# Kernel tuning notes

Hardware: AMD Instinct MI355X
Metric: run time of the kernel (lower is better)

The kernel has to match this reference:

```python
import jax, jax.numpy as jnp
import numpy as np

B, T, D, H = 512, 256, 64, 64  # batch, seq_len, input_dim, hidden_dim


def _lstm_params(key, in_dim, hid):
    k = 1.0 / np.sqrt(hid)
    k1, k2, k3, k4 = jax.random.split(key, 4)
    W_ih = jax.random.uniform(k1, (4 * hid, in_dim), jnp.float32, -k, k)
    W_hh = jax.random.uniform(k2, (4 * hid, hid), jnp.float32, -k, k)
    b_ih = jax.random.uniform(k3, (4 * hid,), jnp.float32, -k, k)
    b_hh = jax.random.uniform(k4, (4 * hid,), jnp.float32, -k, k)
    return W_ih, W_hh, b_ih, b_hh


def setup_inputs() -> dict:
    key = jax.random.key(0)
    ks = jax.random.split(key, 5)
    inp = {"x": jax.random.normal(ks[0], (B, T, D), jnp.float32)}
    names = ["enc0", "enc1", "dec0", "dec1"]
    # encoder: D->H, H->H ; decoder: H->D, D->D (decoder hidden size = input_dim)
    dims = [(D, H), (H, H), (H, D), (D, D)]
    for name, (i, h), k in zip(names, dims, ks[1:]):
        W_ih, W_hh, b_ih, b_hh = _lstm_params(k, i, h)
        inp[f"{name}_Wih"] = W_ih
        inp[f"{name}_Whh"] = W_hh
        inp[f"{name}_bih"] = b_ih
        inp[f"{name}_bhh"] = b_hh
    return inp


def lstm_layer(x, W_ih, W_hh, b_ih, b_hh):
    # x: [B, T, in]; PyTorch gate order: i, f, g, o
    b = x.shape[0]
    h_dim = W_hh.shape[1]
    # precompute input contribution for all timesteps (one big GEMM)
    xg = jnp.einsum('bti,gi->btg', x, W_ih) + b_ih + b_hh  # [B, T, 4H]

    def step(carry, xt):
        h, c = carry
        g = xt + h @ W_hh.T  # [B, 4H]
        i, f, gg, o = jnp.split(g, 4, axis=-1)
        i = jax.nn.sigmoid(i)
        f = jax.nn.sigmoid(f)
        gg = jnp.tanh(gg)
        o = jax.nn.sigmoid(o)
        c = f * c + i * gg
        h = o * jnp.tanh(c)
        return (h, c), h

    h0 = jnp.zeros((b, h_dim), x.dtype)
    (_, _), hs = jax.lax.scan(step, (h0, h0), jnp.swapaxes(xg, 0, 1))
    return jnp.swapaxes(hs, 0, 1)  # [B, T, H]


def reference(x,
              enc0_Wih, enc0_Whh, enc0_bih, enc0_bhh,
              enc1_Wih, enc1_Whh, enc1_bih, enc1_bhh,
              dec0_Wih, dec0_Whh, dec0_bih, dec0_bhh,
              dec1_Wih, dec1_Whh, dec1_bih, dec1_bhh):
    # Eval-mode forward (inter-layer dropout p=0.2 is disabled at inference)
    h = lstm_layer(x, enc0_Wih, enc0_Whh, enc0_bih, enc0_bhh)
    enc = lstm_layer(h, enc1_Wih, enc1_Whh, enc1_bih, enc1_bhh)
    h = lstm_layer(enc, dec0_Wih, dec0_Whh, dec0_bih, dec0_bhh)
    dec = lstm_layer(h, dec1_Wih, dec1_Whh, dec1_bih, dec1_bhh)
    return dec
```

## Files before the change

kernel.cpp:

```cpp
#include <hip/hip_runtime.h>


typedef _Float16 f16x8 __attribute__((ext_vector_type(8)));
typedef float    f32x4 __attribute__((ext_vector_type(4)));

#define TSEQ 256

__device__ __forceinline__ float fast_rcp(float x) { return __builtin_amdgcn_rcpf(x); }
__device__ __forceinline__ float sigm(float x) { return fast_rcp(1.0f + __expf(-x)); }
__device__ __forceinline__ float tanh_fast(float x) {
    return 2.0f * fast_rcp(1.0f + __expf(-2.0f * x)) - 1.0f;
}
__device__ __forceinline__ f16x8 cvt8(float4 a, float4 b) {
    f16x8 f;
    f[0] = (_Float16)a.x; f[1] = (_Float16)a.y; f[2] = (_Float16)a.z; f[3] = (_Float16)a.w;
    f[4] = (_Float16)b.x; f[5] = (_Float16)b.y; f[6] = (_Float16)b.z; f[7] = (_Float16)b.w;
    return f;
}
__device__ __forceinline__ float bperm(int addr, float v) {
    return __int_as_float(__builtin_amdgcn_ds_bpermute(addr, __float_as_int(v)));
}

__global__ __launch_bounds__(512, 2)
void lstm_fused12(const float* __restrict__ x,
                  float* __restrict__ out,
                  const float* __restrict__ Wih0, const float* __restrict__ Whh0,
                  const float* __restrict__ bi0,  const float* __restrict__ bh0,
                  const float* __restrict__ Wih1, const float* __restrict__ Whh1,
                  const float* __restrict__ bi1,  const float* __restrict__ bh1,
                  const float* __restrict__ Wih2, const float* __restrict__ Whh2,
                  const float* __restrict__ bi2,  const float* __restrict__ bh2,
                  const float* __restrict__ Wih3, const float* __restrict__ Whh3,
                  const float* __restrict__ bi3,  const float* __restrict__ bh3)
{
    __shared__ _Float16 Hb[4][4][2][64];
    __shared__ int      Sf[8];

    const int tid  = threadIdx.x;
    const int wave = tid >> 6;
    const int lane = tid & 63;
    const int L    = wave >> 1;
    const int mh   = wave & 1;
    const int q    = lane >> 4;
    const int n    = lane & 15;
    const int b0   = blockIdx.x * 2;

    const float* Wih = (L == 0) ? Wih0 : (L == 1) ? Wih1 : (L == 2) ? Wih2 : Wih3;
    const float* Whh = (L == 0) ? Whh0 : (L == 1) ? Whh1 : (L == 2) ? Whh2 : Whh3;
    const float* bi  = (L == 0) ? bi0  : (L == 1) ? bi1  : (L == 2) ? bi2  : bi3;
    const float* bh  = (L == 0) ? bh0  : (L == 1) ? bh1  : (L == 2) ? bh2  : bh3;

    f16x8 Bih[4][2][2], Bhh[4][2][2];
#pragma unroll
    for (int g = 0; g < 4; ++g) {
#pragma unroll
        for (int s = 0; s < 2; ++s) {
            const int row = g * 64 + mh * 32 + s * 16 + n;
#pragma unroll
            for (int c = 0; c < 2; ++c) {
                const float* pi = Wih + row * 64 + c * 32 + q * 8;
                const float* ph = Whh + row * 64 + c * 32 + q * 8;
                f16x8 fi, fh;
#pragma unroll
                for (int k = 0; k < 8; ++k) { fi[k] = (_Float16)pi[k]; fh[k] = (_Float16)ph[k]; }
                Bih[g][s][c] = fi;
                Bhh[g][s][c] = fh;
            }
        }
    }

    const int eu = lane & 31;
    const int el = lane >> 5;
    const int unit = mh * 32 + eu;
    float4 be;
    be.x = bi[unit]       + bh[unit];
    be.y = bi[64 + unit]  + bh[64 + unit];
    be.z = bi[128 + unit] + bh[128 + unit];
    be.w = bi[192 + unit] + bh[192 + unit];
    float cst = 0.0f;
    float* outp = out + ((size_t)(b0 + el) * TSEQ) * 64 + unit;

    const int baddr = n * 4;

    ((int*)Hb)[tid] = 0;
    ((int*)Hb)[tid + 512] = 0;
    if (tid < 8) Sf[tid] = -2;

    const float* xbase = x + ((size_t)(b0 + (n & 1)) * TSEQ) * 64 + q * 8;
    float4 A0, A1, A2, A3, B0, B1, B2, B3;
    A0 = A1 = A2 = A3 = make_float4(0.f, 0.f, 0.f, 0.f);
    B0 = B1 = B2 = B3 = A0;
    if (L == 0 && n < 2) {
        A0 = *(const float4*)(xbase);      A1 = *(const float4*)(xbase + 4);
        A2 = *(const float4*)(xbase + 32); A3 = *(const float4*)(xbase + 36);
        B0 = *(const float4*)(xbase + 64);  B1 = *(const float4*)(xbase + 68);
        B2 = *(const float4*)(xbase + 96);  B3 = *(const float4*)(xbase + 100);
    }

    __syncthreads();

    const f32x4 z4 = {0.f, 0.f, 0.f, 0.f};
    const int NI = 131;

    for (int i = 0; i < NI; ++i) {
        const bool act = (unsigned)(i - L) < 128u;
        if (act) {
            const int s0 = 2 * (i - L);
            const int s1 = s0 + 1;

            f16x8 vfA0, vfA1, vfB0, vfB1;
            if (L == 0) {
                vfA0 = cvt8(A0, A1);  vfA1 = cvt8(A2, A3);
                vfB0 = cvt8(B0, B1);  vfB1 = cvt8(B2, B3);
                if (s0 + 2 < TSEQ && n < 2) {
                    const float* p = xbase + (size_t)(s0 + 2) * 64;
                    A0 = *(const float4*)(p);      A1 = *(const float4*)(p + 4);
                    A2 = *(const float4*)(p + 32); A3 = *(const float4*)(p + 36);
                    if (s0 + 3 < TSEQ) {
                        B0 = *(const float4*)(p + 64); B1 = *(const float4*)(p + 68);
                        B2 = *(const float4*)(p + 96); B3 = *(const float4*)(p + 100);
                    }
                }
            } else {
                const _Float16* va = &Hb[s0 & 3][L - 1][n & 1][0];
                vfA0 = *(const f16x8*)(va + q * 8);
                vfA1 = *(const f16x8*)(va + 32 + q * 8);
                const _Float16* vb = &Hb[s1 & 3][L - 1][n & 1][0];
                vfB0 = *(const f16x8*)(vb + q * 8);
                vfB1 = *(const f16x8*)(vb + 32 + q * 8);
            }
            const _Float16* hp = &Hb[(s0 - 1) & 3][L][n & 1][0];
            f16x8 hf0 = *(const f16x8*)(hp + q * 8);
            f16x8 hf1 = *(const f16x8*)(hp + 32 + q * 8);

            f32x4 Cgs[2][4];
#pragma unroll
            for (int s = 0; s < 2; ++s) {
#pragma unroll
                for (int g = 0; g < 4; ++g) {
                    f32x4 c;
                    c = __builtin_amdgcn_mfma_f32_16x16x32_f16(hf0, Bhh[g][s][0], z4, 0, 0, 0);
                    c = __builtin_amdgcn_mfma_f32_16x16x32_f16(hf1, Bhh[g][s][1], c,  0, 0, 0);
                    c = __builtin_amdgcn_mfma_f32_16x16x32_f16(vfA0, Bih[g][s][0], c,  0, 0, 0);
                    Cgs[s][g] = __builtin_amdgcn_mfma_f32_16x16x32_f16(vfA1, Bih[g][s][1], c, 0, 0, 0);
                }
            }
            float gv[4];
#pragma unroll
            for (int g = 0; g < 4; ++g) {
                float v00 = bperm(baddr, Cgs[0][g][0]);
                float v10 = bperm(baddr, Cgs[1][g][0]);
                float v01 = bperm(baddr, Cgs[0][g][1]);
                float v11 = bperm(baddr, Cgs[1][g][1]);
                float lo = (q & 1) ? v10 : v00;
                float hi = (q & 1) ? v11 : v01;
                gv[g] = (q & 2) ? hi : lo;
            }
            {
                float gi = sigm(gv[0] + be.x);
                float gf = sigm(gv[1] + be.y);
                float gg = tanh_fast(gv[2] + be.z);
                float go = sigm(gv[3] + be.w);
                cst = gf * cst + gi * gg;
                float h = go * tanh_fast(cst);
                if (L == 3) outp[(size_t)s0 * 64] = h;
                Hb[s0 & 3][L][el][unit] = (_Float16)h;
            }

            asm volatile("s_waitcnt lgkmcnt(0)" ::: "memory");
            if (lane == 0) ((volatile int*)Sf)[wave] = s0;
            for (;;) {
                asm volatile("" ::: "memory");
                int pv = ((volatile int*)Sf)[wave ^ 1];
                if (pv >= s0) break;
                __builtin_amdgcn_s_sleep(1);
            }
            const _Float16* hq = &Hb[s0 & 3][L][n & 1][0];
            f16x8 hg0 = *(const f16x8*)(hq + q * 8);
            f16x8 hg1 = *(const f16x8*)(hq + 32 + q * 8);

#pragma unroll
            for (int s = 0; s < 2; ++s) {
#pragma unroll
                for (int g = 0; g < 4; ++g) {
                    f32x4 c;
                    c = __builtin_amdgcn_mfma_f32_16x16x32_f16(hg0, Bhh[g][s][0], z4, 0, 0, 0);
                    c = __builtin_amdgcn_mfma_f32_16x16x32_f16(hg1, Bhh[g][s][1], c,  0, 0, 0);
                    c = __builtin_amdgcn_mfma_f32_16x16x32_f16(vfB0, Bih[g][s][0], c,  0, 0, 0);
                    Cgs[s][g] = __builtin_amdgcn_mfma_f32_16x16x32_f16(vfB1, Bih[g][s][1], c, 0, 0, 0);
                }
            }
#pragma unroll
            for (int g = 0; g < 4; ++g) {
                float v00 = bperm(baddr, Cgs[0][g][0]);
                float v10 = bperm(baddr, Cgs[1][g][0]);
                float v01 = bperm(baddr, Cgs[0][g][1]);
                float v11 = bperm(baddr, Cgs[1][g][1]);
                float lo = (q & 1) ? v10 : v00;
                float hi = (q & 1) ? v11 : v01;
                gv[g] = (q & 2) ? hi : lo;
            }
            {
                float gi = sigm(gv[0] + be.x);
                float gf = sigm(gv[1] + be.y);
                float gg = tanh_fast(gv[2] + be.z);
                float go = sigm(gv[3] + be.w);
                cst = gf * cst + gi * gg;
                float h = go * tanh_fast(cst);
                if (L == 3) outp[(size_t)s1 * 64] = h;
                Hb[s1 & 3][L][el][unit] = (_Float16)h;
            }
        }
        __builtin_amdgcn_sched_barrier(0);
        asm volatile("s_waitcnt lgkmcnt(0)" ::: "memory");
        __builtin_amdgcn_s_barrier();
        __builtin_amdgcn_sched_barrier(0);
    }
}

extern "C" void kernel_launch(void* const* d_in, const int* in_sizes, int n_in,
                              void* d_out, int out_size, void* d_ws, size_t ws_size,
                              hipStream_t stream) {
    const float* x = (const float*)d_in[0];
    float* out = (float*)d_out;

    lstm_fused12<<<256, 512, 0, stream>>>(
        x, out,
        (const float*)d_in[1],  (const float*)d_in[2],
        (const float*)d_in[3],  (const float*)d_in[4],
        (const float*)d_in[5],  (const float*)d_in[6],
        (const float*)d_in[7],  (const float*)d_in[8],
        (const float*)d_in[9],  (const float*)d_in[10],
        (const float*)d_in[11], (const float*)d_in[12],
        (const float*)d_in[13], (const float*)d_in[14],
        (const float*)d_in[15], (const float*)d_in[16]);
}
```

Measured before the change: 385.4 us.

## Pack both timesteps' input projections into one MFMA pass using spare M rows

The 16-row MFMA tile only used rows 0-1 (two batch rows). Rows 2-3 now carry the second timestep's input, so one set of input-projection MFMAs covers both timesteps. The recurrent term for step s1 is then accumulated onto those rows with only the W_hh MFMAs, and rows 2-3 are read back. This removes the input-projection MFMAs from the second half-step, shortening the serial critical path. The cost is extra lane-select logic, zeroed h operands on the extra rows, and a different accumulation order.

```diff
diff --git a/kernel.cpp b/kernel.cpp
--- a/kernel.cpp
+++ b/kernel.cpp
@@ -22,7 +22,7 @@
 }
 
 __global__ __launch_bounds__(512, 2)
-void lstm_fused12(const float* __restrict__ x,
+void lstm_fused13(const float* __restrict__ x,
                   float* __restrict__ out,
                   const float* __restrict__ Wih0, const float* __restrict__ Whh0,
                   const float* __restrict__ bi0,  const float* __restrict__ bh0,
@@ -44,6 +44,7 @@
     const int q    = lane >> 4;
     const int n    = lane & 15;
     const int b0   = blockIdx.x * 2;
+    const int lsel = (n >> 1) == 1;
 
     const float* Wih = (L == 0) ? Wih0 : (L == 1) ? Wih1 : (L == 2) ? Wih2 : Wih3;
     const float* Whh = (L == 0) ? Whh0 : (L == 1) ? Whh1 : (L == 2) ? Whh2 : Whh3;
@@ -87,14 +88,12 @@
     if (tid < 8) Sf[tid] = -2;
 
     const float* xbase = x + ((size_t)(b0 + (n & 1)) * TSEQ) * 64 + q * 8;
-    float4 A0, A1, A2, A3, B0, B1, B2, B3;
-    A0 = A1 = A2 = A3 = make_float4(0.f, 0.f, 0.f, 0.f);
-    B0 = B1 = B2 = B3 = A0;
-    if (L == 0 && n < 2) {
-        A0 = *(const float4*)(xbase);      A1 = *(const float4*)(xbase + 4);
-        A2 = *(const float4*)(xbase + 32); A3 = *(const float4*)(xbase + 36);
-        B0 = *(const float4*)(xbase + 64);  B1 = *(const float4*)(xbase + 68);
-        B2 = *(const float4*)(xbase + 96);  B3 = *(const float4*)(xbase + 100);
+    float4 R0, R1, R2, R3;
+    R0 = R1 = R2 = R3 = make_float4(0.f, 0.f, 0.f, 0.f);
+    if (L == 0 && n < 4) {
+        const float* p = xbase + (size_t)(n >> 1) * 64;
+        R0 = *(const float4*)(p);      R1 = *(const float4*)(p + 4);
+        R2 = *(const float4*)(p + 32); R3 = *(const float4*)(p + 36);
     }
 
     __syncthreads();
@@ -107,31 +106,36 @@
         if (act) {
             const int s0 = 2 * (i - L);
             const int s1 = s0 + 1;
-
-            f16x8 vfA0, vfA1, vfB0, vfB1;
+            const int p2 = (s0 & 3);
+            const int sprev = (s0 - 1) & 3;
+
+            f16x8 vf0, vf1;
             if (L == 0) {
-                vfA0 = cvt8(A0, A1);  vfA1 = cvt8(A2, A3);
-                vfB0 = cvt8(B0, B1);  vfB1 = cvt8(B2, B3);
-                if (s0 + 2 < TSEQ && n < 2) {
-                    const float* p = xbase + (size_t)(s0 + 2) * 64;
-                    A0 = *(const float4*)(p);      A1 = *(const float4*)(p + 4);
-                    A2 = *(const float4*)(p + 32); A3 = *(const float4*)(p + 36);
-                    if (s0 + 3 < TSEQ) {
-                        B0 = *(const float4*)(p + 64); B1 = *(const float4*)(p + 68);
-                        B2 = *(const float4*)(p + 96); B3 = *(const float4*)(p + 100);
+                vf0 = cvt8(R0, R1);
+                vf1 = cvt8(R2, R3);
+                if (n < 4) {
+                    const int tl = s0 + 2 + (n >> 1);
+                    if (tl < TSEQ) {
+                        const float* p = xbase + (size_t)tl * 64;
+                        R0 = *(const float4*)(p);      R1 = *(const float4*)(p + 4);
+                        R2 = *(const float4*)(p + 32); R3 = *(const float4*)(p + 36);
                     }
                 }
             } else {
-                const _Float16* va = &Hb[s0 & 3][L - 1][n & 1][0];
-                vfA0 = *(const f16x8*)(va + q * 8);
-                vfA1 = *(const f16x8*)(va + 32 + q * 8);
-                const _Float16* vb = &Hb[s1 & 3][L - 1][n & 1][0];
-                vfB0 = *(const f16x8*)(vb + q * 8);
-                vfB1 = *(const f16x8*)(vb + 32 + q * 8);
-            }
-            const _Float16* hp = &Hb[(s0 - 1) & 3][L][n & 1][0];
-            f16x8 hf0 = *(const f16x8*)(hp + q * 8);
-            f16x8 hf1 = *(const f16x8*)(hp + 32 + q * 8);
+                const _Float16* vp = &Hb[p2 + lsel][L - 1][n & 1][0];
+                vf0 = *(const f16x8*)(vp + q * 8);
+                vf1 = *(const f16x8*)(vp + 32 + q * 8);
+            }
+            f16x8 hf0, hf1;
+            {
+                const _Float16* hp = &Hb[sprev][L][n & 1][0];
+                hf0 = *(const f16x8*)(hp + q * 8);
+                hf1 = *(const f16x8*)(hp + 32 + q * 8);
+                if (lsel) {
+#pragma unroll
+                    for (int k = 0; k < 8; ++k) { hf0[k] = (_Float16)0.f; hf1[k] = (_Float16)0.f; }
+                }
+            }
 
             f32x4 Cgs[2][4];
 #pragma unroll
@@ -139,12 +143,13 @@
 #pragma unroll
                 for (int g = 0; g < 4; ++g) {
                     f32x4 c;
-                    c = __builtin_amdgcn_mfma_f32_16x16x32_f16(hf0, Bhh[g][s][0], z4, 0, 0, 0);
-                    c = __builtin_amdgcn_mfma_f32_16x16x32_f16(hf1, Bhh[g][s][1], c,  0, 0, 0);
-                    c = __builtin_amdgcn_mfma_f32_16x16x32_f16(vfA0, Bih[g][s][0], c,  0, 0, 0);
-                    Cgs[s][g] = __builtin_amdgcn_mfma_f32_16x16x32_f16(vfA1, Bih[g][s][1], c, 0, 0, 0);
-                }
-            }
+                    c = __builtin_amdgcn_mfma_f32_16x16x32_f16(vf0, Bih[g][s][0], z4, 0, 0, 0);
+                    c = __builtin_amdgcn_mfma_f32_16x16x32_f16(vf1, Bih[g][s][1], c,  0, 0, 0);
+                    c = __builtin_amdgcn_mfma_f32_16x16x32_f16(hf0, Bhh[g][s][0], c,  0, 0, 0);
+                    Cgs[s][g] = __builtin_amdgcn_mfma_f32_16x16x32_f16(hf1, Bhh[g][s][1], c, 0, 0, 0);
+                }
+            }
+
             float gv[4];
 #pragma unroll
             for (int g = 0; g < 4; ++g) {
@@ -164,7 +169,7 @@
                 cst = gf * cst + gi * gg;
                 float h = go * tanh_fast(cst);
                 if (L == 3) outp[(size_t)s0 * 64] = h;
-                Hb[s0 & 3][L][el][unit] = (_Float16)h;
+                Hb[p2][L][el][unit] = (_Float16)h;
             }
 
             asm volatile("s_waitcnt lgkmcnt(0)" ::: "memory");
@@ -175,7 +180,7 @@
                 if (pv >= s0) break;
                 __builtin_amdgcn_s_sleep(1);
             }
-            const _Float16* hq = &Hb[s0 & 3][L][n & 1][0];
+            const _Float16* hq = &Hb[p2][L][n & 1][0];
             f16x8 hg0 = *(const f16x8*)(hq + q * 8);
             f16x8 hg1 = *(const f16x8*)(hq + 32 + q * 8);
 
@@ -184,18 +189,17 @@
 #pragma unroll
                 for (int g = 0; g < 4; ++g) {
                     f32x4 c;
-                    c = __builtin_amdgcn_mfma_f32_16x16x32_f16(hg0, Bhh[g][s][0], z4, 0, 0, 0);
-                    c = __builtin_amdgcn_mfma_f32_16x16x32_f16(hg1, Bhh[g][s][1], c,  0, 0, 0);
-                    c = __builtin_amdgcn_mfma_f32_16x16x32_f16(vfB0, Bih[g][s][0], c,  0, 0, 0);
-                    Cgs[s][g] = __builtin_amdgcn_mfma_f32_16x16x32_f16(vfB1, Bih[g][s][1], c, 0, 0, 0);
-                }
-            }
+                    c = __builtin_amdgcn_mfma_f32_16x16x32_f16(hg0, Bhh[g][s][0], Cgs[s][g], 0, 0, 0);
+                    Cgs[s][g] = __builtin_amdgcn_mfma_f32_16x16x32_f16(hg1, Bhh[g][s][1], c, 0, 0, 0);
+                }
+            }
+
 #pragma unroll
             for (int g = 0; g < 4; ++g) {
-                float v00 = bperm(baddr, Cgs[0][g][0]);
-                float v10 = bperm(baddr, Cgs[1][g][0]);
-                float v01 = bperm(baddr, Cgs[0][g][1]);
-                float v11 = bperm(baddr, Cgs[1][g][1]);
+                float v00 = bperm(baddr, Cgs[0][g][2]);
+                float v10 = bperm(baddr, Cgs[1][g][2]);
+                float v01 = bperm(baddr, Cgs[0][g][3]);
+                float v11 = bperm(baddr, Cgs[1][g][3]);
                 float lo = (q & 1) ? v10 : v00;
                 float hi = (q & 1) ? v11 : v01;
                 gv[g] = (q & 2) ? hi : lo;
@@ -208,7 +212,7 @@
                 cst = gf * cst + gi * gg;
                 float h = go * tanh_fast(cst);
                 if (L == 3) outp[(size_t)s1 * 64] = h;
-                Hb[s1 & 3][L][el][unit] = (_Float16)h;
+                Hb[p2 + 1][L][el][unit] = (_Float16)h;
             }
         }
         __builtin_amdgcn_sched_barrier(0);
@@ -224,7 +228,7 @@
     const float* x = (const float*)d_in[0];
     float* out = (float*)d_out;
 
-    lstm_fused12<<<256, 512, 0, stream>>>(
+    lstm_fused13<<<256, 512, 0, stream>>>(
         x, out,
         (const float*)d_in[1],  (const float*)d_in[2],
         (const float*)d_in[3],  (const float*)d_in[4],
```

After: 353.7 us. 8.2% less time.
